# Kernel optimization log

Measured on AMD Instinct MI355X. Metric: run time of the kernel, lower is better.

The kernel has to match this reference:

```python
import jax, jax.numpy as jnp
import numpy as np

DIM = 1536      # model dim
NH = 12         # num heads
HD = 128        # head dim
F, H, W = 3, 26, 48   # video latent grid (frames, height, width)
S = F * H * W   # sequence length = 3744
B = 1
EPS = 1e-6
C2 = HD // 2    # 64 rotary pairs per head
SPLITS = [C2 - 2 * (C2 // 3), C2 // 3, C2 // 3]  # [22, 21, 21] for (f, h, w)


def _rope_angles():
    """Wan rope_params: concat of per-axis inverse-frequency angle tables, [1024, 64]."""
    def rp(dim):  # returns [1024, dim//2]
        inv = 1.0 / (10000.0 ** (np.arange(0, dim, 2, dtype=np.float64) / dim))
        return np.outer(np.arange(1024, dtype=np.float64), inv)
    a = np.concatenate([rp(HD - 4 * (HD // 6)), rp(2 * (HD // 6)), rp(2 * (HD // 6))], axis=1)
    return jnp.asarray(a, jnp.float32)


def setup_inputs() -> dict:
    key = jax.random.key(0)
    ks = jax.random.split(key, 9)
    std = DIM ** -0.5
    return {
        "x": jax.random.normal(ks[0], (B, S, DIM), jnp.float32),
        "wq": jax.random.normal(ks[1], (DIM, DIM), jnp.float32) * std,
        "bq": jnp.zeros((DIM,), jnp.float32),
        "wk": jax.random.normal(ks[2], (DIM, DIM), jnp.float32) * std,
        "bk": jnp.zeros((DIM,), jnp.float32),
        "wv": jax.random.normal(ks[3], (DIM, DIM), jnp.float32) * std,
        "bv": jnp.zeros((DIM,), jnp.float32),
        "wo": jax.random.normal(ks[4], (DIM, DIM), jnp.float32) * std,
        "bo": jnp.zeros((DIM,), jnp.float32),
        "gq": jnp.ones((DIM,), jnp.float32),   # WanRMSNorm weight for q
        "gk": jnp.ones((DIM,), jnp.float32),   # WanRMSNorm weight for k
        "freqs": _rope_angles(),                # [1024, 64] rotary angles
        "seq_lens": jnp.full((B,), S, jnp.int32),
    }


def _rmsnorm(y, g):
    return y * jax.lax.rsqrt(jnp.mean(jnp.square(y), axis=-1, keepdims=True) + EPS) * g


def _rope_grid(freqs):
    """Build per-position rotary angles [S, C2] from the 3D grid (F,H,W)."""
    af = freqs[:F, :SPLITS[0]]                       # [F, 22]
    ah = freqs[:H, SPLITS[0]:SPLITS[0] + SPLITS[1]]  # [H, 21]
    aw = freqs[:W, SPLITS[0] + SPLITS[1]:]           # [W, 21]
    ang = jnp.concatenate([
        jnp.broadcast_to(af[:, None, None, :], (F, H, W, SPLITS[0])),
        jnp.broadcast_to(ah[None, :, None, :], (F, H, W, SPLITS[1])),
        jnp.broadcast_to(aw[None, None, :, :], (F, H, W, SPLITS[2])),
    ], axis=-1)
    return ang.reshape(S, C2)


def _rope_apply(t, cos, sin):
    # t: [B, S, NH, HD]; pairs (even, odd) rotated by angle.
    tp = t.reshape(B, S, NH, C2, 2)
    xr, xi = tp[..., 0], tp[..., 1]
    yr = xr * cos - xi * sin
    yi = xr * sin + xi * cos
    return jnp.stack([yr, yi], axis=-1).reshape(B, S, NH, HD)


def reference(x, wq, bq, wk, bk, wv, bv, wo, bo, gq, gk, freqs, seq_lens):
    q = _rmsnorm(x @ wq.T + bq, gq).reshape(B, S, NH, HD)
    k = _rmsnorm(x @ wk.T + bk, gk).reshape(B, S, NH, HD)
    v = (x @ wv.T + bv).reshape(B, S, NH, HD)

    ang = _rope_grid(freqs)                    # [S, C2]
    cos = jnp.cos(ang)[None, :, None, :]       # [1, S, 1, C2]
    sin = jnp.sin(ang)[None, :, None, :]
    q = _rope_apply(q, cos, sin)
    k = _rope_apply(k, cos, sin)

    scale = HD ** -0.5
    scores = jnp.einsum('bqhd,bkhd->bhqk', q, k) * scale   # [B, NH, S, S]
    kmask = jnp.arange(S)[None, :] < seq_lens[:, None]     # [B, S]
    scores = jnp.where(kmask[:, None, None, :], scores, jnp.float32(-1e9))
    attn = jax.nn.softmax(scores, axis=-1)
    out = jnp.einsum('bhqk,bkhd->bqhd', attn, v).reshape(B, S, DIM)
    return out @ wo.T + bo
```

## Files before the change

### kernel.cpp

```cpp
#include <hip/hip_runtime.h>
#include <stdint.h>


#define DIM   1536
#define S_TOT 3744
#define NHEAD 12
#define HD    128

using short8 = __attribute__((ext_vector_type(8))) short;
using f32x4  = __attribute__((ext_vector_type(4))) float;
using f32x2  = __attribute__((ext_vector_type(2))) float;

__device__ __forceinline__ unsigned short f2bf(float f) {
  unsigned u = __builtin_bit_cast(unsigned, f);
  u += 0x7fffu + ((u >> 16) & 1u);
  return (unsigned short)(u >> 16);
}

__device__ __forceinline__ void gl_lds16(const void* g, void* l) {
  auto gp = (const __attribute__((address_space(1))) unsigned int*)g;
  auto lp = (__attribute__((address_space(3))) unsigned int*)(uintptr_t)l;
  __builtin_amdgcn_global_load_lds(gp, lp, 16, 0, 0);
}

#define NX4 (S_TOT * DIM / 4)
#define NW4 (DIM * DIM / 4)
__global__ __launch_bounds__(256) void cvt5_kernel(
    const float* __restrict__ x, const float* __restrict__ wq,
    const float* __restrict__ wk, const float* __restrict__ wv,
    const float* __restrict__ wo,
    unsigned short* __restrict__ xb, unsigned short* __restrict__ wqb,
    unsigned short* __restrict__ wkb, unsigned short* __restrict__ wvb,
    unsigned short* __restrict__ wob) {
  int gid = blockIdx.x * 256 + threadIdx.x;
  const float* src; unsigned short* dst; int off;
  if (gid < NX4)                { src = x;  dst = xb;  off = gid; }
  else if (gid < NX4 + NW4)     { src = wq; dst = wqb; off = gid - NX4; }
  else if (gid < NX4 + 2 * NW4) { src = wk; dst = wkb; off = gid - NX4 - NW4; }
  else if (gid < NX4 + 3 * NW4) { src = wv; dst = wvb; off = gid - NX4 - 2 * NW4; }
  else if (gid < NX4 + 4 * NW4) { src = wo; dst = wob; off = gid - NX4 - 3 * NW4; }
  else return;
  float4 v = ((const float4*)src)[off];
  ushort4 o;
  o.x = f2bf(v.x); o.y = f2bf(v.y); o.z = f2bf(v.z); o.w = f2bf(v.w);
  ((ushort4*)dst)[off] = o;
}

__device__ __forceinline__ void gemm_body(const unsigned short* __restrict__ A,
                                          const unsigned short* __restrict__ W,
                                          const float* __restrict__ bias,
                                          float* __restrict__ outF,
                                          unsigned short* __restrict__ outB,
                                          int M, int mode) {
  constexpr int K = DIM, N = DIM;
  __shared__ unsigned short As[128 * 32];
  __shared__ unsigned short Ws[128 * 32];
  int tid = threadIdx.x;
  int w = tid >> 6, lane = tid & 63;
  int wr = w >> 1, wc = w & 1, q4 = lane >> 4, ql = lane & 15;
  int m0 = blockIdx.y * 128, n0 = blockIdx.x * 128;

  f32x4 acc[4][4];
  const f32x4 zero4 = {0.f, 0.f, 0.f, 0.f};
#pragma unroll
  for (int i = 0; i < 4; i++)
#pragma unroll
    for (int j = 0; j < 4; j++) acc[i][j] = zero4;

  for (int k0 = 0; k0 < K; k0 += 32) {
    __syncthreads();
#pragma unroll
    for (int r = 0; r < 2; r++) {
      int idx = r * 256 + tid;
      int row = idx >> 2, ch = idx & 3;
      int am = m0 + row; am = (am < M) ? am : (M - 1);
      gl_lds16(A + (size_t)am * K + k0 + ch * 8, &As[idx * 8]);
      gl_lds16(W + (size_t)(n0 + row) * K + k0 + ch * 8, &Ws[idx * 8]);
    }
    __syncthreads();
    short8 af[4], wf[4];
#pragma unroll
    for (int i = 0; i < 4; i++)
      af[i] = *(const short8*)&As[(wr * 64 + i * 16 + ql) * 32 + q4 * 8];
#pragma unroll
    for (int j = 0; j < 4; j++)
      wf[j] = *(const short8*)&Ws[(wc * 64 + j * 16 + ql) * 32 + q4 * 8];
#pragma unroll
    for (int i = 0; i < 4; i++)
#pragma unroll
      for (int j = 0; j < 4; j++)
        acc[i][j] = __builtin_amdgcn_mfma_f32_16x16x32_bf16(af[i], wf[j], acc[i][j], 0, 0, 0);
  }

  float bb[4];
#pragma unroll
  for (int j = 0; j < 4; j++) bb[j] = bias[n0 + wc * 64 + j * 16 + ql];
#pragma unroll
  for (int i = 0; i < 4; i++) {
#pragma unroll
    for (int rg = 0; rg < 4; rg++) {
      int row = m0 + wr * 64 + i * 16 + q4 * 4 + rg;
      if (row < M) {
#pragma unroll
        for (int j = 0; j < 4; j++) {
          int col = n0 + wc * 64 + j * 16 + ql;
          float v = acc[i][j][rg] + bb[j];
          if (mode == 0) outF[(size_t)row * N + col] = v;
          else           outB[(size_t)row * N + col] = f2bf(v);
        }
      }
    }
  }
}

__global__ __launch_bounds__(256) void gemm_qkv_kernel(
    const unsigned short* __restrict__ xb,
    const unsigned short* __restrict__ wqb, const unsigned short* __restrict__ wkb,
    const unsigned short* __restrict__ wvb,
    const float* __restrict__ bq, const float* __restrict__ bk, const float* __restrict__ bv,
    float* __restrict__ Yq, float* __restrict__ Yk, unsigned short* __restrict__ Vb) {
  int z = blockIdx.z;
  const unsigned short* W = (z == 0) ? wqb : ((z == 1) ? wkb : wvb);
  const float* bias       = (z == 0) ? bq  : ((z == 1) ? bk  : bv);
  float* outF             = (z == 0) ? Yq  : Yk;
  gemm_body(xb, W, bias, outF, Vb, S_TOT, (z == 2) ? 1 : 0);
}

__global__ __launch_bounds__(256) void gemm_out_kernel(
    const unsigned short* __restrict__ AO, const unsigned short* __restrict__ wob,
    const float* __restrict__ bo, float* __restrict__ out) {
  gemm_body(AO, wob, bo, out, nullptr, S_TOT, 0);
}

__global__ __launch_bounds__(256) void normrope_kernel(
    const float* __restrict__ Yq, const float* __restrict__ Yk,
    const float* __restrict__ gq, const float* __restrict__ gk,
    const float* __restrict__ freqs,
    unsigned short* __restrict__ Qb, unsigned short* __restrict__ Kb) {
  int s = blockIdx.x;
  int tid = threadIdx.x;
  int w = tid >> 6, lane = tid & 63;
  const f32x2* yq2 = (const f32x2*)(Yq + (size_t)s * DIM);
  const f32x2* yk2 = (const f32x2*)(Yk + (size_t)s * DIM);
  f32x2 vq[3], vk[3];
  float ssq = 0.f, ssk = 0.f;
#pragma unroll
  for (int r = 0; r < 3; r++) {
    int p = tid + 256 * r;
    vq[r] = yq2[p]; vk[r] = yk2[p];
    ssq += vq[r].x * vq[r].x + vq[r].y * vq[r].y;
    ssk += vk[r].x * vk[r].x + vk[r].y * vk[r].y;
  }
#pragma unroll
  for (int d = 1; d < 64; d <<= 1) {
    ssq += __shfl_xor(ssq, d);
    ssk += __shfl_xor(ssk, d);
  }
  __shared__ float rq[4], rk[4];
  if (lane == 0) { rq[w] = ssq; rk[w] = ssk; }
  __syncthreads();
  float tq = rq[0] + rq[1] + rq[2] + rq[3];
  float tk = rk[0] + rk[1] + rk[2] + rk[3];
  float invq = rsqrtf(tq * (1.f / DIM) + 1e-6f);
  float invk = rsqrtf(tk * (1.f / DIM) + 1e-6f);

  int fi = s / (26 * 48);
  int hi = (s / 48) % 26;
  int wi = s % 48;
#pragma unroll
  for (int r = 0; r < 3; r++) {
    int p = tid + 256 * r;
    int c = p & 63;
    int frow = (c < 22) ? fi : ((c < 43) ? hi : wi);
    float ang = freqs[frow * 64 + c];
    float sn, cs;
    __sincosf(ang, &sn, &cs);
    {
      float a = vq[r].x * invq * gq[2 * p];
      float b = vq[r].y * invq * gq[2 * p + 1];
      ushort2 o; o.x = f2bf(a * cs - b * sn); o.y = f2bf(a * sn + b * cs);
      ((ushort2*)Qb)[(size_t)s * (DIM / 2) + p] = o;
    }
    {
      float a = vk[r].x * invk * gk[2 * p];
      float b = vk[r].y * invk * gk[2 * p + 1];
      ushort2 o; o.x = f2bf(a * cs - b * sn); o.y = f2bf(a * sn + b * cs);
      ((ushort2*)Kb)[(size_t)s * (DIM / 2) + p] = o;
    }
  }
}

__global__ __launch_bounds__(256) void vtrans_kernel(const unsigned short* __restrict__ Vb,
                                                     unsigned short* __restrict__ Vt) {
  int d0 = blockIdx.x * 64, s0 = blockIdx.y * 64;
  __shared__ unsigned short t[64][65];
  int tid = threadIdx.x;
#pragma unroll
  for (int r = 0; r < 4; r++) {
    int idx = r * 256 + tid;
    int sr = idx >> 4, c4 = (idx & 15) * 4;
    ushort4 v; v.x = v.y = v.z = v.w = 0;
    int s = s0 + sr;
    if (s < S_TOT) v = *(const ushort4*)(Vb + (size_t)s * DIM + d0 + c4);
    t[sr][c4 + 0] = v.x; t[sr][c4 + 1] = v.y; t[sr][c4 + 2] = v.z; t[sr][c4 + 3] = v.w;
  }
  __syncthreads();
#pragma unroll
  for (int r = 0; r < 4; r++) {
    int idx = r * 256 + tid;
    int dr = idx >> 4, s4 = (idx & 15) * 4;
    if (s0 + s4 < S_TOT) {
      ushort4 v;
      v.x = t[s4 + 0][dr]; v.y = t[s4 + 1][dr]; v.z = t[s4 + 2][dr]; v.w = t[s4 + 3][dr];
      *(ushort4*)(Vt + (size_t)(d0 + dr) * S_TOT + s0 + s4) = v;
    }
  }
}

__global__ __launch_bounds__(256, 3) void attn_kernel(
    const unsigned short* __restrict__ Qb, const unsigned short* __restrict__ Kb,
    const unsigned short* __restrict__ Vt, unsigned short* __restrict__ AO,
    const int* __restrict__ seq_lens) {
  int h = blockIdx.y;
  int tid = threadIdx.x;
  int w = tid >> 6, lane = tid & 63;
  int q4 = lane >> 4, ql = lane & 15;
  int seqlen = seq_lens[0]; if (seqlen > S_TOT) seqlen = S_TOT;

  __shared__ unsigned short Kl[64 * 128];
  __shared__ unsigned short Vl[128 * 64];
  __shared__ unsigned short Pl[4][16 * 72];

  int q0 = blockIdx.x * 64 + w * 16;
  bool wact = (q0 < S_TOT);

  short8 qf[4];
  {
    int qrow = q0 + ql; if (qrow > S_TOT - 1) qrow = S_TOT - 1;
#pragma unroll
    for (int ks = 0; ks < 4; ks++)
      qf[ks] = *(const short8*)(Qb + (size_t)qrow * DIM + h * HD + ks * 32 + q4 * 8);
  }

  f32x4 o[8];
  const f32x4 zero4 = {0.f, 0.f, 0.f, 0.f};
#pragma unroll
  for (int nt = 0; nt < 8; nt++) o[nt] = zero4;
  float m_run = -3.0e38f, l_run = 0.f;
  const float sm_l2 = 0.08838834764831845f * 1.4426950408889634f;

  const size_t hoff = (size_t)h * HD;

  for (int kt = 0; kt < (S_TOT + 63) / 64; kt++) {
    int k0 = kt * 64;
    __syncthreads();
    {
      const unsigned short* kseg = Kb + (size_t)k0 * DIM + hoff;
#pragma unroll
      for (int r = 0; r < 4; r++) {
        int idx = r * 256 + tid;
        int row = idx >> 4, c = idx & 15;
        int g = c ^ (row & 15);
        gl_lds16(kseg + (size_t)row * DIM + g * 8, &Kl[idx * 8]);
      }
      int kmax = S_TOT - 8 - k0;
#pragma unroll
      for (int r = 0; r < 4; r++) {
        int idx = r * 256 + tid;
        int row = idx >> 3, c = idx & 7;
        int g = c ^ (row & 7);
        int kc = g * 8; if (kc > kmax) kc = kmax;
        gl_lds16(Vt + (hoff + row) * S_TOT + k0 + kc, &Vl[idx * 8]);
      }
    }
    __syncthreads();
    if (!wact) continue;

    f32x4 st[4];
#pragma unroll
    for (int mt = 0; mt < 4; mt++) {
      st[mt] = zero4;
#pragma unroll
      for (int ks = 0; ks < 4; ks++) {
        int c = (ks * 4 + q4) ^ ql;
        short8 kf = *(const short8*)&Kl[(mt * 16 + ql) * 128 + c * 8];
        st[mt] = __builtin_amdgcn_mfma_f32_16x16x32_bf16(kf, qf[ks], st[mt], 0, 0, 0);
      }
    }

    float sc[16];
#pragma unroll
    for (int mt = 0; mt < 4; mt++)
#pragma unroll
      for (int rg = 0; rg < 4; rg++)
        sc[mt * 4 + rg] = st[mt][rg] * sm_l2;
    if (k0 + 64 > seqlen) {
#pragma unroll
      for (int mt = 0; mt < 4; mt++)
#pragma unroll
        for (int rg = 0; rg < 4; rg++) {
          int key = k0 + mt * 16 + q4 * 4 + rg;
          if (key >= seqlen) sc[mt * 4 + rg] = -3.0e38f;
        }
    }
    float mloc = -3.0e38f;
#pragma unroll
    for (int i = 0; i < 16; i++) mloc = fmaxf(mloc, sc[i]);
    mloc = fmaxf(mloc, __shfl_xor(mloc, 16));
    mloc = fmaxf(mloc, __shfl_xor(mloc, 32));

    if (!__all(mloc <= m_run + 8.0f)) {
      float mnew = fmaxf(m_run, mloc);
      float alpha = exp2f(m_run - mnew);
      m_run = mnew;
      l_run *= alpha;
      float ar[4];
#pragma unroll
      for (int rg = 0; rg < 4; rg++) ar[rg] = __shfl(alpha, q4 * 4 + rg, 16);
#pragma unroll
      for (int nt = 0; nt < 8; nt++)
#pragma unroll
        for (int rg = 0; rg < 4; rg++) o[nt][rg] *= ar[rg];
    }

    float lloc = 0.f;
#pragma unroll
    for (int mt = 0; mt < 4; mt++) {
      float p0 = exp2f(sc[mt * 4 + 0] - m_run);
      float p1 = exp2f(sc[mt * 4 + 1] - m_run);
      float p2 = exp2f(sc[mt * 4 + 2] - m_run);
      float p3 = exp2f(sc[mt * 4 + 3] - m_run);
      lloc += p0 + p1 + p2 + p3;
      ushort4 pk;
      pk.x = f2bf(p0); pk.y = f2bf(p1); pk.z = f2bf(p2); pk.w = f2bf(p3);
      *(ushort4*)&Pl[w][ql * 72 + mt * 16 + q4 * 4] = pk;
    }
    lloc += __shfl_xor(lloc, 16);
    lloc += __shfl_xor(lloc, 32);
    l_run += lloc;

#pragma unroll
    for (int ks2 = 0; ks2 < 2; ks2++) {
      short8 pa = *(const short8*)&Pl[w][ql * 72 + ks2 * 32 + q4 * 8];
#pragma unroll
      for (int nt = 0; nt < 8; nt++) {
        int c = (ks2 * 4 + q4) ^ (ql & 7);
        short8 vb = *(const short8*)&Vl[(nt * 16 + ql) * 64 + c * 8];
        o[nt] = __builtin_amdgcn_mfma_f32_16x16x32_bf16(pa, vb, o[nt], 0, 0, 0);
      }
    }
  }

  if (wact) {
    float il = 1.0f / l_run;
    float ilr[4];
#pragma unroll
    for (int rg = 0; rg < 4; rg++) ilr[rg] = __shfl(il, q4 * 4 + rg, 16);
#pragma unroll
    for (int rg = 0; rg < 4; rg++) {
      int row = q0 + q4 * 4 + rg;
      if (row < S_TOT) {
#pragma unroll
        for (int nt = 0; nt < 8; nt++)
          AO[(size_t)row * DIM + h * HD + nt * 16 + ql] = f2bf(o[nt][rg] * ilr[rg]);
      }
    }
  }
}

extern "C" void kernel_launch(void* const* d_in, const int* in_sizes, int n_in,
                              void* d_out, int out_size, void* d_ws, size_t ws_size,
                              hipStream_t stream) {
  const float* x    = (const float*)d_in[0];
  const float* wq   = (const float*)d_in[1];
  const float* bq   = (const float*)d_in[2];
  const float* wk   = (const float*)d_in[3];
  const float* bk   = (const float*)d_in[4];
  const float* wv   = (const float*)d_in[5];
  const float* bv   = (const float*)d_in[6];
  const float* wo   = (const float*)d_in[7];
  const float* bo   = (const float*)d_in[8];
  const float* gq   = (const float*)d_in[9];
  const float* gk   = (const float*)d_in[10];
  const float* freqs = (const float*)d_in[11];
  const int*   seq  = (const int*)d_in[12];

  char* ws = (char*)d_ws;
  const size_t SZ_X = (size_t)S_TOT * DIM * 2;
  const size_t SZ_W = (size_t)DIM * DIM * 2;
  const size_t SZ_Y = (size_t)S_TOT * DIM * 4;

  unsigned short* xb  = (unsigned short*)(ws);
  unsigned short* wqb = (unsigned short*)(ws + SZ_X);
  unsigned short* wkb = (unsigned short*)(ws + SZ_X + SZ_W);
  unsigned short* wvb = (unsigned short*)(ws + SZ_X + 2 * SZ_W);
  unsigned short* wob = (unsigned short*)(ws + SZ_X + 3 * SZ_W);
  float*          Yq  = (float*)(ws + SZ_X + 4 * SZ_W);
  float*          Yk  = (float*)(ws + SZ_X + 4 * SZ_W + SZ_Y);
  unsigned short* Vb  = (unsigned short*)(ws + SZ_X + 4 * SZ_W + 2 * SZ_Y);
  unsigned short* Qb  = (unsigned short*)(ws + SZ_X + 4 * SZ_W + 2 * SZ_Y + SZ_X);
  unsigned short* Kb  = (unsigned short*)(ws + SZ_X + 4 * SZ_W + 2 * SZ_Y + 2 * SZ_X);
  unsigned short* Vt  = (unsigned short*)(ws + SZ_X + 4 * SZ_W + 2 * SZ_Y + 3 * SZ_X);
  unsigned short* AO  = (unsigned short*)(ws + SZ_X + 4 * SZ_W + 2 * SZ_Y + 4 * SZ_X);

  int total4 = NX4 + 4 * NW4;
  cvt5_kernel<<<dim3((total4 + 255) / 256), 256, 0, stream>>>(
      x, wq, wk, wv, wo, xb, wqb, wkb, wvb, wob);

  gemm_qkv_kernel<<<dim3(DIM / 128, (S_TOT + 127) / 128, 3), 256, 0, stream>>>(
      xb, wqb, wkb, wvb, bq, bk, bv, Yq, Yk, Vb);

  normrope_kernel<<<dim3(S_TOT), 256, 0, stream>>>(Yq, Yk, gq, gk, freqs, Qb, Kb);

  vtrans_kernel<<<dim3(DIM / 64, (S_TOT + 63) / 64), 256, 0, stream>>>(Vb, Vt);

  attn_kernel<<<dim3((S_TOT + 63) / 64, NHEAD), 256, 0, stream>>>(Qb, Kb, Vt, AO, seq);

  gemm_out_kernel<<<dim3(DIM / 128, (S_TOT + 127) / 128), 256, 0, stream>>>(
      AO, wob, bo, (float*)d_out);
}
```

Before: 426.8 us.

## Double-buffer attention K/V tiles with 32-key steps and XCD-aware block mapping

Restructures the attention main loop to use 32-key tiles staged into double-buffered LDS with async global-to-LDS loads and partial vmcnt waits, so the next tile's loads overlap the current tile's MFMA work. The softmax scale is folded into the Q RMSNorm factor, removing a multiply per score. Workgroups are remapped so each XCD gets contiguous query tiles of the same head, which is meant to improve L2 reuse of K/V. It also uses packed bf16 conversion instructions and s_setprio around the MFMA blocks. Smaller tiles double the loop-iteration and barrier count and make the online-softmax rescale check run more often. Correctness now depends on S_TOT being a multiple of 32 (3744 is), since the V column clamp was removed.

```diff
diff --git a/kernel.cpp b/kernel.cpp
--- a/kernel.cpp
+++ b/kernel.cpp
@@ -6,6 +6,8 @@
 #define S_TOT 3744
 #define NHEAD 12
 #define HD    128
+#define QT    59
+#define NT    117
 
 using short8 = __attribute__((ext_vector_type(8))) short;
 using f32x4  = __attribute__((ext_vector_type(4))) float;
@@ -161,7 +163,8 @@
   __syncthreads();
   float tq = rq[0] + rq[1] + rq[2] + rq[3];
   float tk = rk[0] + rk[1] + rk[2] + rk[3];
-  float invq = rsqrtf(tq * (1.f / DIM) + 1e-6f);
+  const float SM_L2 = 0.08838834764831845f * 1.4426950408889634f;
+  float invq = rsqrtf(tq * (1.f / DIM) + 1e-6f) * SM_L2;
   float invk = rsqrtf(tk * (1.f / DIM) + 1e-6f);
 
   int fi = s / (26 * 48);
@@ -221,91 +224,112 @@
     const unsigned short* __restrict__ Qb, const unsigned short* __restrict__ Kb,
     const unsigned short* __restrict__ Vt, unsigned short* __restrict__ AO,
     const int* __restrict__ seq_lens) {
-  int h = blockIdx.y;
+  const int NWG = QT * NHEAD;
+  int bid = blockIdx.x;
+  int xcd = bid & 7, bix = bid >> 3;
+  const int qc = NWG >> 3, rr = NWG & 7;
+  int wg = (xcd < rr ? xcd * (qc + 1) : rr * (qc + 1) + (xcd - rr) * qc) + bix;
+  int h  = wg / QT;
+  int qt = wg - h * QT;
+
   int tid = threadIdx.x;
   int w = tid >> 6, lane = tid & 63;
   int q4 = lane >> 4, ql = lane & 15;
   int seqlen = seq_lens[0]; if (seqlen > S_TOT) seqlen = S_TOT;
 
-  __shared__ unsigned short Kl[64 * 128];
-  __shared__ unsigned short Vl[128 * 64];
-  __shared__ unsigned short Pl[4][16 * 72];
-
-  int q0 = blockIdx.x * 64 + w * 16;
+  __shared__ unsigned short Kl[2][32 * 128];
+  __shared__ unsigned short Vl[2][128 * 32];
+  __shared__ unsigned short Pl[4][16 * 40];
+
+  int q0 = qt * 64 + w * 16;
   bool wact = (q0 < S_TOT);
+
+  const size_t hoff = (size_t)h * HD;
+
+  auto stage = [&](int buf, int t) {
+    int k0 = t * 32;
+    const unsigned short* kseg = Kb + (size_t)k0 * DIM + hoff;
+#pragma unroll
+    for (int r = 0; r < 2; r++) {
+      int idx = r * 256 + tid;
+      int row = idx >> 4, c = idx & 15;
+      int g = c ^ (row & 15);
+      gl_lds16(kseg + (size_t)row * DIM + g * 8, &Kl[buf][idx * 8]);
+    }
+#pragma unroll
+    for (int r = 0; r < 2; r++) {
+      int idx = r * 256 + tid;
+      int row = idx >> 2, c = idx & 3;
+      int g = c ^ (row & 3);
+      gl_lds16(Vt + (hoff + row) * S_TOT + k0 + g * 8, &Vl[buf][idx * 8]);
+    }
+  };
 
   short8 qf[4];
   {
     int qrow = q0 + ql; if (qrow > S_TOT - 1) qrow = S_TOT - 1;
 #pragma unroll
     for (int ks = 0; ks < 4; ks++)
-      qf[ks] = *(const short8*)(Qb + (size_t)qrow * DIM + h * HD + ks * 32 + q4 * 8);
-  }
+      qf[ks] = *(const short8*)(Qb + (size_t)qrow * DIM + hoff + ks * 32 + q4 * 8);
+  }
+  asm volatile("s_waitcnt vmcnt(0)" ::: "memory");
 
   f32x4 o[8];
   const f32x4 zero4 = {0.f, 0.f, 0.f, 0.f};
 #pragma unroll
   for (int nt = 0; nt < 8; nt++) o[nt] = zero4;
   float m_run = -3.0e38f, l_run = 0.f;
-  const float sm_l2 = 0.08838834764831845f * 1.4426950408889634f;
-
-  const size_t hoff = (size_t)h * HD;
-
-  for (int kt = 0; kt < (S_TOT + 63) / 64; kt++) {
-    int k0 = kt * 64;
-    __syncthreads();
-    {
-      const unsigned short* kseg = Kb + (size_t)k0 * DIM + hoff;
-#pragma unroll
-      for (int r = 0; r < 4; r++) {
-        int idx = r * 256 + tid;
-        int row = idx >> 4, c = idx & 15;
-        int g = c ^ (row & 15);
-        gl_lds16(kseg + (size_t)row * DIM + g * 8, &Kl[idx * 8]);
-      }
-      int kmax = S_TOT - 8 - k0;
-#pragma unroll
-      for (int r = 0; r < 4; r++) {
-        int idx = r * 256 + tid;
-        int row = idx >> 3, c = idx & 7;
-        int g = c ^ (row & 7);
-        int kc = g * 8; if (kc > kmax) kc = kmax;
-        gl_lds16(Vt + (hoff + row) * S_TOT + k0 + kc, &Vl[idx * 8]);
-      }
-    }
-    __syncthreads();
+
+  stage(0, 0);
+
+  for (int t = 0; t < NT; ++t) {
+    int cur = t & 1;
+    int k0 = t * 32;
+    __builtin_amdgcn_s_barrier();
+    asm volatile("" ::: "memory");
+    if (t + 1 < NT) {
+      stage(cur ^ 1, t + 1);
+      asm volatile("s_waitcnt vmcnt(4)" ::: "memory");
+    } else {
+      asm volatile("s_waitcnt vmcnt(0)" ::: "memory");
+    }
+    __builtin_amdgcn_sched_barrier(0);
+    __builtin_amdgcn_s_barrier();
+    asm volatile("" ::: "memory");
     if (!wact) continue;
 
-    f32x4 st[4];
-#pragma unroll
-    for (int mt = 0; mt < 4; mt++) {
+    f32x4 st[2];
+    __builtin_amdgcn_s_setprio(1);
+#pragma unroll
+    for (int mt = 0; mt < 2; mt++) {
       st[mt] = zero4;
 #pragma unroll
       for (int ks = 0; ks < 4; ks++) {
         int c = (ks * 4 + q4) ^ ql;
-        short8 kf = *(const short8*)&Kl[(mt * 16 + ql) * 128 + c * 8];
+        short8 kf = *(const short8*)&Kl[cur][(mt * 16 + ql) * 128 + c * 8];
         st[mt] = __builtin_amdgcn_mfma_f32_16x16x32_bf16(kf, qf[ks], st[mt], 0, 0, 0);
       }
     }
-
-    float sc[16];
-#pragma unroll
-    for (int mt = 0; mt < 4; mt++)
+    __builtin_amdgcn_s_setprio(0);
+
+    float sc[8];
+#pragma unroll
+    for (int mt = 0; mt < 2; mt++)
 #pragma unroll
       for (int rg = 0; rg < 4; rg++)
-        sc[mt * 4 + rg] = st[mt][rg] * sm_l2;
-    if (k0 + 64 > seqlen) {
-#pragma unroll
-      for (int mt = 0; mt < 4; mt++)
+        sc[mt * 4 + rg] = st[mt][rg];
+    if (k0 + 32 > seqlen) {
+#pragma unroll
+      for (int mt = 0; mt < 2; mt++)
 #pragma unroll
         for (int rg = 0; rg < 4; rg++) {
           int key = k0 + mt * 16 + q4 * 4 + rg;
           if (key >= seqlen) sc[mt * 4 + rg] = -3.0e38f;
         }
     }
-    float mloc = -3.0e38f;
-#pragma unroll
-    for (int i = 0; i < 16; i++) mloc = fmaxf(mloc, sc[i]);
+    float mloc = sc[0];
+#pragma unroll
+    for (int i = 1; i < 8; i++) mloc = fmaxf(mloc, sc[i]);
     mloc = fmaxf(mloc, __shfl_xor(mloc, 16));
     mloc = fmaxf(mloc, __shfl_xor(mloc, 32));
 
@@ -325,30 +349,31 @@
 
     float lloc = 0.f;
 #pragma unroll
-    for (int mt = 0; mt < 4; mt++) {
+    for (int mt = 0; mt < 2; mt++) {
       float p0 = exp2f(sc[mt * 4 + 0] - m_run);
       float p1 = exp2f(sc[mt * 4 + 1] - m_run);
       float p2 = exp2f(sc[mt * 4 + 2] - m_run);
       float p3 = exp2f(sc[mt * 4 + 3] - m_run);
       lloc += p0 + p1 + p2 + p3;
-      ushort4 pk;
-      pk.x = f2bf(p0); pk.y = f2bf(p1); pk.z = f2bf(p2); pk.w = f2bf(p3);
-      *(ushort4*)&Pl[w][ql * 72 + mt * 16 + q4 * 4] = pk;
+      unsigned pk0, pk1;
+      asm("v_cvt_pk_bf16_f32 %0, %1, %2" : "=v"(pk0) : "v"(p0), "v"(p1));
+      asm("v_cvt_pk_bf16_f32 %0, %1, %2" : "=v"(pk1) : "v"(p2), "v"(p3));
+      uint2 pw; pw.x = pk0; pw.y = pk1;
+      *(uint2*)&Pl[w][ql * 40 + mt * 16 + q4 * 4] = pw;
     }
     lloc += __shfl_xor(lloc, 16);
     lloc += __shfl_xor(lloc, 32);
     l_run += lloc;
 
-#pragma unroll
-    for (int ks2 = 0; ks2 < 2; ks2++) {
-      short8 pa = *(const short8*)&Pl[w][ql * 72 + ks2 * 32 + q4 * 8];
-#pragma unroll
-      for (int nt = 0; nt < 8; nt++) {
-        int c = (ks2 * 4 + q4) ^ (ql & 7);
-        short8 vb = *(const short8*)&Vl[(nt * 16 + ql) * 64 + c * 8];
-        o[nt] = __builtin_amdgcn_mfma_f32_16x16x32_bf16(pa, vb, o[nt], 0, 0, 0);
-      }
-    }
+    short8 pa = *(const short8*)&Pl[w][ql * 40 + q4 * 8];
+    __builtin_amdgcn_s_setprio(1);
+#pragma unroll
+    for (int nt = 0; nt < 8; nt++) {
+      int c = q4 ^ (ql & 3);
+      short8 vb = *(const short8*)&Vl[cur][(nt * 16 + ql) * 32 + c * 8];
+      o[nt] = __builtin_amdgcn_mfma_f32_16x16x32_bf16(pa, vb, o[nt], 0, 0, 0);
+    }
+    __builtin_amdgcn_s_setprio(0);
   }
 
   if (wact) {
@@ -362,7 +387,7 @@
       if (row < S_TOT) {
 #pragma unroll
         for (int nt = 0; nt < 8; nt++)
-          AO[(size_t)row * DIM + h * HD + nt * 16 + ql] = f2bf(o[nt][rg] * ilr[rg]);
+          AO[(size_t)row * DIM + hoff + nt * 16 + ql] = f2bf(o[nt][rg] * ilr[rg]);
       }
     }
   }
@@ -414,7 +439,7 @@
 
   vtrans_kernel<<<dim3(DIM / 64, (S_TOT + 63) / 64), 256, 0, stream>>>(Vb, Vt);
 
-  attn_kernel<<<dim3((S_TOT + 63) / 64, NHEAD), 256, 0, stream>>>(Qb, Kb, Vt, AO, seq);
+  attn_kernel<<<dim3(QT * NHEAD), 256, 0, stream>>>(Qb, Kb, Vt, AO, seq);
 
   gemm_out_kernel<<<dim3(DIM / 128, (S_TOT + 127) / 128), 256, 0, stream>>>(
       AO, wob, bo, (float*)d_out);
```

After: 428.5 us. About the same (+0.4%).
